# Kernel optimization log

Hardware: AMD Instinct MI355X
Metric: run time of the kernel (lower is better)

The kernel has to match this reference:

```python
import jax, jax.numpy as jnp
import numpy as np

N = 8192
D_IN = 3
D_K = 128
HID = 256
N_RES = 2
N_TRI = 2730
N_EDGE = 2048
EPS = float(jnp.finfo(jnp.float32).eps)  # torch RMSNorm default eps=None -> finfo eps


def setup_inputs() -> dict:
    key = jax.random.key(0)
    ks = jax.random.split(key, 16)
    std = 0.02
    inp = {
        "edge_features": jax.random.normal(ks[0], (N, D_IN), dtype=jnp.float32),
        "edge_ids": jax.random.randint(ks[1], (N,), 0, N_EDGE),
        "triangle_ids": jax.random.randint(ks[2], (N,), 0, N_TRI),
        # projections (stored as [in, out]; equivalent to torch Linear)
        "Wq": jax.random.normal(ks[3], (D_IN, D_K), dtype=jnp.float32) * std,
        "bq": jnp.zeros((D_K,), jnp.float32),
        "Wk": jax.random.normal(ks[4], (D_IN, D_K), dtype=jnp.float32) * std,
        "bk": jnp.zeros((D_K,), jnp.float32),
        "Wv": jax.random.normal(ks[5], (D_IN, D_K), dtype=jnp.float32) * std,
        "bv": jnp.zeros((D_K,), jnp.float32),
        # attention MLP: Linear(d_k, hid) -> N_RES ResBlocks -> Linear(hid, 1)
        "W0": jax.random.normal(ks[6], (D_K, HID), dtype=jnp.float32) * std,
        "b0": jnp.zeros((HID,), jnp.float32),
        "rms_w": jnp.ones((N_RES, HID), jnp.float32),
        "Wres": jax.random.normal(ks[7], (N_RES, HID, HID), dtype=jnp.float32) * std,
        "bres": jnp.zeros((N_RES, HID), jnp.float32),
        "Wout": jax.random.normal(ks[8], (HID, 1), dtype=jnp.float32) * std,
        "bout": jnp.zeros((1,), jnp.float32),
    }
    return inp


def _rmsnorm(x, g):
    ms = jnp.mean(x * x, axis=-1, keepdims=True)
    return x * jax.lax.rsqrt(ms + EPS) * g


def reference(edge_features, edge_ids, triangle_ids,
              Wq, bq, Wk, bk, Wv, bv,
              W0, b0, rms_w, Wres, bres, Wout, bout):
    q = edge_features @ Wq + bq          # [N, d_k]
    k = edge_features @ Wk + bk
    v = edge_features @ Wv + bv
    scores = (q @ k.T) / jnp.sqrt(jnp.float32(D_K))   # [N, N]
    mask = triangle_ids[:, None] == triangle_ids[None, :]
    scores = jnp.where(mask, scores, -jnp.inf)
    attn = jax.nn.softmax(scores, axis=1)             # every row has diag True
    attended = attn @ v                                # [N, d_k]
    # MLP with ResBlocks
    h = attended @ W0 + b0                             # [N, hid]
    for i in range(N_RES):
        h = h + jax.nn.relu(_rmsnorm(h, rms_w[i]) @ Wres[i] + bres[i])
    logits = (h @ Wout + bout)[:, 0]                   # [N]
    # scatter_softmax over edge_ids (dim=0)
    seg_max = jax.ops.segment_max(logits, edge_ids, num_segments=N_EDGE)
    ex = jnp.exp(logits - seg_max[edge_ids])
    seg_sum = jax.ops.segment_sum(ex, edge_ids, num_segments=N_EDGE)
    weights = ex / seg_sum[edge_ids]
    return weights
```

## Files before the change

### kernel.cpp

```cpp
#include <hip/hip_runtime.h>
#include <math.h>

#define N 8192
#define D_IN 3
#define D_K 128
#define HID 256
#define N_RES 2
#define N_TRI 2730
#define N_EDGE 2048
#define EPS 1.1920929e-07f

typedef unsigned short u16;
typedef unsigned int u32;
typedef float f32x4 __attribute__((ext_vector_type(4)));
typedef short s16x8 __attribute__((ext_vector_type(8)));

#define OFF_LOGITS   0
#define OFF_TRIOFF   32768
#define OFF_TRICNT   43776
#define OFF_MEMT     54784
#define OFF_EOFF     87552
#define OFF_ECNT     95744
#define OFF_MEME     103936
#define OFF_WPK      136704

__device__ __forceinline__ u16 f2bf(float f) {
    u32 u = __float_as_uint(f);
    u32 r = (u + 0x7fffu + ((u >> 16) & 1u)) >> 16;
    return (u16)r;
}
__device__ __forceinline__ u32 pack2bf(float a, float b) {
    return (u32)f2bf(a) | ((u32)f2bf(b) << 16);
}

__global__ __launch_bounds__(1024) void k_setup(
        const int* __restrict__ tri, const int* __restrict__ eids,
        const float* __restrict__ W0, const float* __restrict__ Wres,
        int* __restrict__ tri_off, int* __restrict__ tri_cnt, int* __restrict__ mem_t,
        int* __restrict__ e_off, int* __restrict__ e_cnt, int* __restrict__ mem_e,
        u16* __restrict__ Wpk) {
    if (blockIdx.x != 0) {
        int tg = (blockIdx.x - 1) * 1024 + threadIdx.x;
        int tile = tg >> 6, lane = tg & 63;
        int q = lane >> 4, c = lane & 15;
        u16 tmp[8];
        int dst;
        if (tile < 64) {
            int nt = tile >> 2, kt = tile & 3;
            int k0 = kt * 32 + q * 8, n = nt * 16 + c;
            dst = (tile * 64 + lane) * 8;
            #pragma unroll
            for (int j = 0; j < 8; ++j) tmp[j] = f2bf(W0[(k0 + j) * HID + n]);
        } else {
            int t2 = tile - 64;
            int r = t2 >> 7, tl = t2 & 127;
            int nt = tl >> 3, kt = tl & 7;
            int k0 = kt * 32 + q * 8, n = nt * 16 + c;
            dst = 32768 + r * 65536 + (tl * 64 + lane) * 8;
            const float* W = Wres + r * 65536;
            #pragma unroll
            for (int j = 0; j < 8; ++j) tmp[j] = f2bf(W[(k0 + j) * HID + n]);
        }
        *(s16x8*)&Wpk[dst] = *(s16x8*)tmp;
        return;
    }
    __shared__ int sc[4096];
    __shared__ int ec[2048];
    __shared__ int wp[16];
    const int t = threadIdx.x, lane = t & 63, wid = t >> 6;
    for (int i = t; i < 4096; i += 1024) sc[i] = 0;
    for (int i = t; i < 2048; i += 1024) ec[i] = 0;
    __syncthreads();
    for (int n = t; n < N; n += 1024) {
        atomicAdd(&sc[tri[n]], 1);
        atomicAdd(&ec[eids[n]], 1);
    }
    __syncthreads();
    int a0 = sc[t*4], a1 = sc[t*4+1], a2 = sc[t*4+2], a3 = sc[t*4+3];
    int c0 = a0, c1 = c0 + a1, c2 = c1 + a2, c3 = c2 + a3;
    int ts = c3;
    #pragma unroll
    for (int o = 1; o < 64; o <<= 1) { int u = __shfl_up(ts, o); if (lane >= o) ts += u; }
    if (lane == 63) wp[wid] = ts;
    __syncthreads();
    if (wid == 0) {
        int v = (lane < 16) ? wp[lane] : 0;
        #pragma unroll
        for (int o = 1; o < 16; o <<= 1) { int u = __shfl_up(v, o); if (lane >= o) v += u; }
        if (lane < 16) wp[lane] = v;
    }
    __syncthreads();
    {
        int wexcl = wid ? wp[wid - 1] : 0;
        int texcl = wexcl + ts - c3;
        int o0 = texcl, o1 = texcl + c0, o2 = texcl + c1, o3 = texcl + c2;
        if (t*4+0 < N_TRI) { tri_off[t*4+0] = o0; tri_cnt[t*4+0] = a0; }
        if (t*4+1 < N_TRI) { tri_off[t*4+1] = o1; tri_cnt[t*4+1] = a1; }
        if (t*4+2 < N_TRI) { tri_off[t*4+2] = o2; tri_cnt[t*4+2] = a2; }
        if (t*4+3 < N_TRI) { tri_off[t*4+3] = o3; tri_cnt[t*4+3] = a3; }
        sc[t*4+0] = o0; sc[t*4+1] = o1; sc[t*4+2] = o2; sc[t*4+3] = o3;
    }
    __syncthreads();
    int ea0 = ec[t*2], ea1 = ec[t*2+1];
    int f0 = ea0, f1 = f0 + ea1;
    int es = f1;
    #pragma unroll
    for (int o = 1; o < 64; o <<= 1) { int u = __shfl_up(es, o); if (lane >= o) es += u; }
    if (lane == 63) wp[wid] = es;
    __syncthreads();
    if (wid == 0) {
        int v = (lane < 16) ? wp[lane] : 0;
        #pragma unroll
        for (int o = 1; o < 16; o <<= 1) { int u = __shfl_up(v, o); if (lane >= o) v += u; }
        if (lane < 16) wp[lane] = v;
    }
    __syncthreads();
    {
        int wexcl = wid ? wp[wid - 1] : 0;
        int texcl = wexcl + es - f1;
        int eo0 = texcl, eo1 = texcl + f0;
        e_off[t*2+0] = eo0; e_cnt[t*2+0] = ea0;
        e_off[t*2+1] = eo1; e_cnt[t*2+1] = ea1;
        ec[t*2+0] = eo0; ec[t*2+1] = eo1;
    }
    __syncthreads();
    for (int n = t; n < N; n += 1024) {
        int p = atomicAdd(&sc[tri[n]], 1);
        mem_t[p] = n;
        int q2 = atomicAdd(&ec[eids[n]], 1);
        mem_e[q2] = n;
    }
}

__global__ __launch_bounds__(512) void k_fused(
        const float* __restrict__ ef, const int* __restrict__ tri,
        const float* __restrict__ Wq, const float* __restrict__ bq,
        const float* __restrict__ Wk, const float* __restrict__ bk,
        const float* __restrict__ Wv, const float* __restrict__ bv,
        const int* __restrict__ tri_off, const int* __restrict__ tri_cnt,
        const int* __restrict__ mem_t,
        const float* __restrict__ b0, const float* __restrict__ rms_w,
        const float* __restrict__ bres, const float* __restrict__ Wout,
        const float* __restrict__ bout, const u16* __restrict__ Wpk,
        float* __restrict__ logits) {
    __shared__ u16 X[16][264];
    __shared__ float red[8][16];
    const int tid = threadIdx.x;
    const int w = tid >> 6, lane = tid & 63;
    const int q = lane >> 4, c = lane & 15;
    const int base = blockIdx.x * 16;
    const int colb = w * 32 + c;

    {
        const int d0 = lane * 2, d1 = d0 + 1;
        float wq0a = Wq[d0], wq1a = Wq[D_K + d0], wq2a = Wq[2*D_K + d0], bqa = bq[d0];
        float wq0b = Wq[d1], wq1b = Wq[D_K + d1], wq2b = Wq[2*D_K + d1], bqb = bq[d1];
        float wk0a = Wk[d0], wk1a = Wk[D_K + d0], wk2a = Wk[2*D_K + d0], bka = bk[d0];
        float wk0b = Wk[d1], wk1b = Wk[D_K + d1], wk2b = Wk[2*D_K + d1], bkb = bk[d1];
        float wv0a = Wv[d0], wv1a = Wv[D_K + d0], wv2a = Wv[2*D_K + d0], bva = bv[d0];
        float wv0b = Wv[d1], wv1b = Wv[D_K + d1], wv2b = Wv[2*D_K + d1], bvb = bv[d1];
        const float scale = 0.08838834764831845f;

        #pragma unroll
        for (int rr = 0; rr < 2; ++rr) {
            int lrow = 2 * w + rr;
            int row = base + lrow;
            float e0 = ef[row*3+0], e1 = ef[row*3+1], e2 = ef[row*3+2];
            float qa = bqa + e0*wq0a + e1*wq1a + e2*wq2a;
            float qb = bqb + e0*wq0b + e1*wq1b + e2*wq2b;
            int tt = tri[row];
            int off = tri_off[tt], cnt = tri_cnt[tt];
            float m = -INFINITY, l = 0.f, acca = 0.f, accb = 0.f;
            for (int bs = 0; bs < cnt; bs += 64) {
                int nn = cnt - bs; if (nn > 64) nn = 64;
                float g0 = 0.f, g1 = 0.f, g2 = 0.f;
                if (lane < nn) {
                    int j = mem_t[off + bs + lane];
                    g0 = ef[j*3+0]; g1 = ef[j*3+1]; g2 = ef[j*3+2];
                }
                for (int ii = 0; ii < nn; ++ii) {
                    float h0 = __shfl(g0, ii), h1 = __shfl(g1, ii), h2 = __shfl(g2, ii);
                    float ka = bka + h0*wk0a + h1*wk1a + h2*wk2a;
                    float kb = bkb + h0*wk0b + h1*wk1b + h2*wk2b;
                    float p = qa * ka + qb * kb;
                    #pragma unroll
                    for (int o = 32; o > 0; o >>= 1) p += __shfl_xor(p, o);
                    float s = p * scale;
                    float va = bva + h0*wv0a + h1*wv1a + h2*wv2a;
                    float vb = bvb + h0*wv0b + h1*wv1b + h2*wv2b;
                    float mn = fmaxf(m, s);
                    float rs = expf(m - mn);
                    float ws = expf(s - mn);
                    l    = l * rs + ws;
                    acca = acca * rs + ws * va;
                    accb = accb * rs + ws * vb;
                    m = mn;
                }
            }
            float inv = 1.f / l;
            *(u32*)&X[lrow][d0] = pack2bf(acca * inv, accb * inv);
        }
    }
    __syncthreads();

    const s16x8* Bp = (const s16x8*)Wpk;
    float h[2][4];
    f32x4 acc[2];
    const f32x4 zero = {0.f, 0.f, 0.f, 0.f};

    #pragma unroll
    for (int nt = 0; nt < 2; ++nt) acc[nt] = zero;
    #pragma unroll
    for (int kt = 0; kt < 4; ++kt) {
        s16x8 a = *(const s16x8*)&X[c][kt * 32 + q * 8];
        #pragma unroll
        for (int nt = 0; nt < 2; ++nt) {
            s16x8 b = Bp[((w * 2 + nt) * 4 + kt) * 64 + lane];
            acc[nt] = __builtin_amdgcn_mfma_f32_16x16x32_bf16(a, b, acc[nt], 0, 0, 0);
        }
    }
    #pragma unroll
    for (int nt = 0; nt < 2; ++nt) {
        float bb = b0[colb + nt * 16];
        #pragma unroll
        for (int rg = 0; rg < 4; ++rg) h[nt][rg] = acc[nt][rg] + bb;
    }

    for (int ir = 0; ir < N_RES; ++ir) {
        float part[4];
        #pragma unroll
        for (int rg = 0; rg < 4; ++rg) {
            part[rg] = h[0][rg] * h[0][rg] + h[1][rg] * h[1][rg];
            #pragma unroll
            for (int o = 1; o < 16; o <<= 1) part[rg] += __shfl_xor(part[rg], o);
        }
        if (c == 0) {
            #pragma unroll
            for (int rg = 0; rg < 4; ++rg) red[w][q * 4 + rg] = part[rg];
        }
        __syncthreads();
        float sc4[4];
        #pragma unroll
        for (int rg = 0; rg < 4; ++rg) {
            int rr = q * 4 + rg;
            float ms = (red[0][rr] + red[1][rr] + red[2][rr] + red[3][rr]
                      + red[4][rr] + red[5][rr] + red[6][rr] + red[7][rr]) * (1.f / HID);
            sc4[rg] = rsqrtf(ms + EPS);
        }
        #pragma unroll
        for (int nt = 0; nt < 2; ++nt) {
            float gg = rms_w[ir * HID + colb + nt * 16];
            #pragma unroll
            for (int rg = 0; rg < 4; ++rg)
                X[q * 4 + rg][colb + nt * 16] = f2bf(h[nt][rg] * sc4[rg] * gg);
        }
        __syncthreads();

        const s16x8* Br = Bp + 4096 + ir * 8192;
        #pragma unroll
        for (int nt = 0; nt < 2; ++nt) acc[nt] = zero;
        #pragma unroll
        for (int kt = 0; kt < 8; ++kt) {
            s16x8 a = *(const s16x8*)&X[c][kt * 32 + q * 8];
            #pragma unroll
            for (int nt = 0; nt < 2; ++nt) {
                s16x8 b = Br[((w * 2 + nt) * 8 + kt) * 64 + lane];
                acc[nt] = __builtin_amdgcn_mfma_f32_16x16x32_bf16(a, b, acc[nt], 0, 0, 0);
            }
        }
        #pragma unroll
        for (int nt = 0; nt < 2; ++nt) {
            float bb = bres[ir * HID + colb + nt * 16];
            #pragma unroll
            for (int rg = 0; rg < 4; ++rg) h[nt][rg] += fmaxf(acc[nt][rg] + bb, 0.f);
        }
    }

    {
        float wo0 = Wout[colb], wo1 = Wout[colb + 16];
        float part[4];
        #pragma unroll
        for (int rg = 0; rg < 4; ++rg) {
            part[rg] = h[0][rg] * wo0 + h[1][rg] * wo1;
            #pragma unroll
            for (int o = 1; o < 16; o <<= 1) part[rg] += __shfl_xor(part[rg], o);
        }
        if (c == 0) {
            #pragma unroll
            for (int rg = 0; rg < 4; ++rg) red[w][q * 4 + rg] = part[rg];
        }
        __syncthreads();
        if (tid < 16) {
            float s = bout[0];
            #pragma unroll
            for (int w2 = 0; w2 < 8; ++w2) s += red[w2][tid];
            logits[base + tid] = s;
        }
    }
}

__global__ __launch_bounds__(256) void k_segsoft(
        const float* __restrict__ logits, const int* __restrict__ e_off,
        const int* __restrict__ e_cnt, const int* __restrict__ mem_e,
        float* __restrict__ out) {
    int e = (blockIdx.x * 256 + threadIdx.x) >> 6;
    int lane = threadIdx.x & 63;
    int off = e_off[e], cnt = e_cnt[e];
    float mx = -INFINITY;
    for (int i = lane; i < cnt; i += 64) mx = fmaxf(mx, logits[mem_e[off + i]]);
    #pragma unroll
    for (int o = 32; o > 0; o >>= 1) mx = fmaxf(mx, __shfl_xor(mx, o));
    float s = 0.f;
    for (int i = lane; i < cnt; i += 64) s += expf(logits[mem_e[off + i]] - mx);
    #pragma unroll
    for (int o = 32; o > 0; o >>= 1) s += __shfl_xor(s, o);
    float inv = 1.f / s;
    for (int i = lane; i < cnt; i += 64) {
        int m = mem_e[off + i];
        out[m] = expf(logits[m] - mx) * inv;
    }
}

extern "C" void kernel_launch(void* const* d_in, const int* in_sizes, int n_in,
                              void* d_out, int out_size, void* d_ws, size_t ws_size,
                              hipStream_t stream) {
    const float* ef   = (const float*)d_in[0];
    const int*   eids = (const int*)d_in[1];
    const int*   tri  = (const int*)d_in[2];
    const float* Wq = (const float*)d_in[3];
    const float* bq = (const float*)d_in[4];
    const float* Wk = (const float*)d_in[5];
    const float* bk = (const float*)d_in[6];
    const float* Wv = (const float*)d_in[7];
    const float* bv = (const float*)d_in[8];
    const float* W0 = (const float*)d_in[9];
    const float* b0 = (const float*)d_in[10];
    const float* rms_w = (const float*)d_in[11];
    const float* Wres  = (const float*)d_in[12];
    const float* bres  = (const float*)d_in[13];
    const float* Wout  = (const float*)d_in[14];
    const float* bout  = (const float*)d_in[15];
    float* out = (float*)d_out;

    char* ws = (char*)d_ws;
    float* logits  = (float*)(ws + OFF_LOGITS);
    int*   tri_off = (int*)(ws + OFF_TRIOFF);
    int*   tri_cnt = (int*)(ws + OFF_TRICNT);
    int*   mem_t   = (int*)(ws + OFF_MEMT);
    int*   e_off   = (int*)(ws + OFF_EOFF);
    int*   e_cnt   = (int*)(ws + OFF_ECNT);
    int*   mem_e   = (int*)(ws + OFF_MEME);
    u16*   Wpk     = (u16*)(ws + OFF_WPK);

    hipLaunchKernelGGL(k_setup, dim3(21), dim3(1024), 0, stream,
                       tri, eids, W0, Wres,
                       tri_off, tri_cnt, mem_t, e_off, e_cnt, mem_e, Wpk);
    hipLaunchKernelGGL(k_fused, dim3(N / 16), dim3(512), 0, stream,
                       ef, tri, Wq, bq, Wk, bk, Wv, bv,
                       tri_off, tri_cnt, mem_t,
                       b0, rms_w, bres, Wout, bout, Wpk, logits);
    hipLaunchKernelGGL(k_segsoft, dim3(N_EDGE / 4), dim3(256), 0, stream,
                       logits, e_off, e_cnt, mem_e, out);
}
```

Baseline: 120.0 us.

## Fold Q/K/V and W0 projections into low-rank precomputed constants

Because D_IN is 3, the attention score reduces to a 3x3 bilinear form, and attn@v@W0 reduces to averaging the 3-dim edge features and then applying a precomputed 3x256 matrix. The setup kernel now computes these small matrices (Wq·Wkᵀ terms, Wv·W0, and the folded bias). The fused kernel then runs attention in 3 dimensions using 32-lane halves with per-chunk softmax and no per-element 64-lane reductions, and replaces the first MFMA GEMM with a rank-3 FMA. This removes most of the attention ALU and shuffle work. It changes rounding, since the first layer now runs in fp32 instead of bf16.

```diff
diff --git a/kernel.cpp b/kernel.cpp
--- a/kernel.cpp
+++ b/kernel.cpp
@@ -23,44 +23,71 @@
 #define OFF_ECNT     95744
 #define OFF_MEME     103936
 #define OFF_WPK      136704
+#define OFF_WV0      398848
+#define OFF_B0P      401920
+#define OFF_ATTC     402944
 
 __device__ __forceinline__ u16 f2bf(float f) {
     u32 u = __float_as_uint(f);
     u32 r = (u + 0x7fffu + ((u >> 16) & 1u)) >> 16;
     return (u16)r;
 }
-__device__ __forceinline__ u32 pack2bf(float a, float b) {
-    return (u32)f2bf(a) | ((u32)f2bf(b) << 16);
-}
 
 __global__ __launch_bounds__(1024) void k_setup(
         const int* __restrict__ tri, const int* __restrict__ eids,
-        const float* __restrict__ W0, const float* __restrict__ Wres,
+        const float* __restrict__ Wq, const float* __restrict__ bq,
+        const float* __restrict__ Wk, const float* __restrict__ bk,
+        const float* __restrict__ Wv, const float* __restrict__ bv,
+        const float* __restrict__ W0, const float* __restrict__ b0,
+        const float* __restrict__ Wres,
         int* __restrict__ tri_off, int* __restrict__ tri_cnt, int* __restrict__ mem_t,
         int* __restrict__ e_off, int* __restrict__ e_cnt, int* __restrict__ mem_e,
-        u16* __restrict__ Wpk) {
+        u16* __restrict__ Wpk, float* __restrict__ Wv0, float* __restrict__ b0p,
+        float* __restrict__ attc) {
+    if (blockIdx.x == 17) {
+        int t = threadIdx.x;
+        if (t < 256) {
+            float a0 = 0.f, a1 = 0.f, a2 = 0.f, ab = 0.f;
+            for (int d = 0; d < D_K; ++d) {
+                float wc = W0[d * HID + t];
+                a0 += Wv[d] * wc;
+                a1 += Wv[D_K + d] * wc;
+                a2 += Wv[2 * D_K + d] * wc;
+                ab += bv[d] * wc;
+            }
+            Wv0[t] = a0; Wv0[256 + t] = a1; Wv0[512 + t] = a2;
+            b0p[t] = ab + b0[t];
+        } else if (t < 272) {
+            int idx = t - 256;
+            float acc = 0.f;
+            if (idx < 9) {
+                int a = idx / 3, b = idx % 3;
+                for (int d = 0; d < D_K; ++d) acc += Wq[a * D_K + d] * Wk[b * D_K + d];
+            } else if (idx < 12) {
+                int a = idx - 9;
+                for (int d = 0; d < D_K; ++d) acc += Wq[a * D_K + d] * bk[d];
+            } else if (idx < 15) {
+                int b = idx - 12;
+                for (int d = 0; d < D_K; ++d) acc += bq[d] * Wk[b * D_K + d];
+            } else {
+                for (int d = 0; d < D_K; ++d) acc += bq[d] * bk[d];
+            }
+            attc[idx] = acc;
+        }
+        return;
+    }
     if (blockIdx.x != 0) {
         int tg = (blockIdx.x - 1) * 1024 + threadIdx.x;
         int tile = tg >> 6, lane = tg & 63;
         int q = lane >> 4, c = lane & 15;
+        int r = tile >> 7, tl = tile & 127;
+        int nt = tl >> 3, kt = tl & 7;
+        int k0 = kt * 32 + q * 8, n = nt * 16 + c;
+        const float* W = Wres + r * 65536;
         u16 tmp[8];
-        int dst;
-        if (tile < 64) {
-            int nt = tile >> 2, kt = tile & 3;
-            int k0 = kt * 32 + q * 8, n = nt * 16 + c;
-            dst = (tile * 64 + lane) * 8;
-            #pragma unroll
-            for (int j = 0; j < 8; ++j) tmp[j] = f2bf(W0[(k0 + j) * HID + n]);
-        } else {
-            int t2 = tile - 64;
-            int r = t2 >> 7, tl = t2 & 127;
-            int nt = tl >> 3, kt = tl & 7;
-            int k0 = kt * 32 + q * 8, n = nt * 16 + c;
-            dst = 32768 + r * 65536 + (tl * 64 + lane) * 8;
-            const float* W = Wres + r * 65536;
-            #pragma unroll
-            for (int j = 0; j < 8; ++j) tmp[j] = f2bf(W[(k0 + j) * HID + n]);
-        }
+        #pragma unroll
+        for (int j = 0; j < 8; ++j) tmp[j] = f2bf(W[(k0 + j) * HID + n]);
+        int dst = r * 65536 + (tl * 64 + lane) * 8;
         *(s16x8*)&Wpk[dst] = *(s16x8*)tmp;
         return;
     }
@@ -134,17 +161,16 @@
 
 __global__ __launch_bounds__(512) void k_fused(
         const float* __restrict__ ef, const int* __restrict__ tri,
-        const float* __restrict__ Wq, const float* __restrict__ bq,
-        const float* __restrict__ Wk, const float* __restrict__ bk,
-        const float* __restrict__ Wv, const float* __restrict__ bv,
         const int* __restrict__ tri_off, const int* __restrict__ tri_cnt,
         const int* __restrict__ mem_t,
-        const float* __restrict__ b0, const float* __restrict__ rms_w,
+        const float* __restrict__ attc, const float* __restrict__ Wv0,
+        const float* __restrict__ b0p, const float* __restrict__ rms_w,
         const float* __restrict__ bres, const float* __restrict__ Wout,
         const float* __restrict__ bout, const u16* __restrict__ Wpk,
         float* __restrict__ logits) {
     __shared__ u16 X[16][264];
     __shared__ float red[8][16];
+    __shared__ float ebar[16][4];
     const int tid = threadIdx.x;
     const int w = tid >> 6, lane = tid & 63;
     const int q = lane >> 4, c = lane & 15;
@@ -152,53 +178,53 @@
     const int colb = w * 32 + c;
 
     {
-        const int d0 = lane * 2, d1 = d0 + 1;
-        float wq0a = Wq[d0], wq1a = Wq[D_K + d0], wq2a = Wq[2*D_K + d0], bqa = bq[d0];
-        float wq0b = Wq[d1], wq1b = Wq[D_K + d1], wq2b = Wq[2*D_K + d1], bqb = bq[d1];
-        float wk0a = Wk[d0], wk1a = Wk[D_K + d0], wk2a = Wk[2*D_K + d0], bka = bk[d0];
-        float wk0b = Wk[d1], wk1b = Wk[D_K + d1], wk2b = Wk[2*D_K + d1], bkb = bk[d1];
-        float wv0a = Wv[d0], wv1a = Wv[D_K + d0], wv2a = Wv[2*D_K + d0], bva = bv[d0];
-        float wv0b = Wv[d1], wv1b = Wv[D_K + d1], wv2b = Wv[2*D_K + d1], bvb = bv[d1];
         const float scale = 0.08838834764831845f;
-
-        #pragma unroll
-        for (int rr = 0; rr < 2; ++rr) {
-            int lrow = 2 * w + rr;
-            int row = base + lrow;
-            float e0 = ef[row*3+0], e1 = ef[row*3+1], e2 = ef[row*3+2];
-            float qa = bqa + e0*wq0a + e1*wq1a + e2*wq2a;
-            float qb = bqb + e0*wq0b + e1*wq1b + e2*wq2b;
-            int tt = tri[row];
-            int off = tri_off[tt], cnt = tri_cnt[tt];
-            float m = -INFINITY, l = 0.f, acca = 0.f, accb = 0.f;
-            for (int bs = 0; bs < cnt; bs += 64) {
-                int nn = cnt - bs; if (nn > 64) nn = 64;
-                float g0 = 0.f, g1 = 0.f, g2 = 0.f;
-                if (lane < nn) {
-                    int j = mem_t[off + bs + lane];
-                    g0 = ef[j*3+0]; g1 = ef[j*3+1]; g2 = ef[j*3+2];
-                }
-                for (int ii = 0; ii < nn; ++ii) {
-                    float h0 = __shfl(g0, ii), h1 = __shfl(g1, ii), h2 = __shfl(g2, ii);
-                    float ka = bka + h0*wk0a + h1*wk1a + h2*wk2a;
-                    float kb = bkb + h0*wk0b + h1*wk1b + h2*wk2b;
-                    float p = qa * ka + qb * kb;
-                    #pragma unroll
-                    for (int o = 32; o > 0; o >>= 1) p += __shfl_xor(p, o);
-                    float s = p * scale;
-                    float va = bva + h0*wv0a + h1*wv1a + h2*wv2a;
-                    float vb = bvb + h0*wv0b + h1*wv1b + h2*wv2b;
-                    float mn = fmaxf(m, s);
-                    float rs = expf(m - mn);
-                    float ws = expf(s - mn);
-                    l    = l * rs + ws;
-                    acca = acca * rs + ws * va;
-                    accb = accb * rs + ws * vb;
-                    m = mn;
-                }
-            }
+        const int half = lane >> 5;
+        const int i = lane & 31;
+        const int lrow = 2 * w + half;
+        const int row = base + lrow;
+        float e0 = ef[row*3+0], e1 = ef[row*3+1], e2 = ef[row*3+2];
+        float t0 = (e0*attc[0] + e1*attc[3] + e2*attc[6] + attc[12]) * scale;
+        float t1 = (e0*attc[1] + e1*attc[4] + e2*attc[7] + attc[13]) * scale;
+        float t2 = (e0*attc[2] + e1*attc[5] + e2*attc[8] + attc[14]) * scale;
+        float tb = (e0*attc[9] + e1*attc[10] + e2*attc[11] + attc[15]) * scale;
+        int tt = tri[row];
+        int off = tri_off[tt], cnt = tri_cnt[tt];
+        float m = -INFINITY, l = 0.f, sa0 = 0.f, sa1 = 0.f, sa2 = 0.f;
+        for (int bs = 0; bs < cnt; bs += 32) {
+            int nn = cnt - bs; if (nn > 32) nn = 32;
+            float f0 = 0.f, f1 = 0.f, f2 = 0.f, s = -INFINITY;
+            if (i < nn) {
+                int j = mem_t[off + bs + i];
+                f0 = ef[j*3+0]; f1 = ef[j*3+1]; f2 = ef[j*3+2];
+                s = tb + t0*f0 + t1*f1 + t2*f2;
+            }
+            float m1 = s;
+            #pragma unroll
+            for (int o = 16; o > 0; o >>= 1) m1 = fmaxf(m1, __shfl_xor(m1, o));
+            float p = (i < nn) ? __expf(s - m1) : 0.f;
+            float pl = p, p0 = p * f0, p1 = p * f1, p2 = p * f2;
+            #pragma unroll
+            for (int o = 16; o > 0; o >>= 1) {
+                pl += __shfl_xor(pl, o);
+                p0 += __shfl_xor(p0, o);
+                p1 += __shfl_xor(p1, o);
+                p2 += __shfl_xor(p2, o);
+            }
+            float mn = fmaxf(m, m1);
+            float ra = __expf(m - mn);
+            float rb = __expf(m1 - mn);
+            l   = l   * ra + pl * rb;
+            sa0 = sa0 * ra + p0 * rb;
+            sa1 = sa1 * ra + p1 * rb;
+            sa2 = sa2 * ra + p2 * rb;
+            m = mn;
+        }
+        if (i == 0) {
             float inv = 1.f / l;
-            *(u32*)&X[lrow][d0] = pack2bf(acca * inv, accb * inv);
+            ebar[lrow][0] = sa0 * inv;
+            ebar[lrow][1] = sa1 * inv;
+            ebar[lrow][2] = sa2 * inv;
         }
     }
     __syncthreads();
@@ -209,21 +235,14 @@
     const f32x4 zero = {0.f, 0.f, 0.f, 0.f};
 
     #pragma unroll
-    for (int nt = 0; nt < 2; ++nt) acc[nt] = zero;
-    #pragma unroll
-    for (int kt = 0; kt < 4; ++kt) {
-        s16x8 a = *(const s16x8*)&X[c][kt * 32 + q * 8];
-        #pragma unroll
-        for (int nt = 0; nt < 2; ++nt) {
-            s16x8 b = Bp[((w * 2 + nt) * 4 + kt) * 64 + lane];
-            acc[nt] = __builtin_amdgcn_mfma_f32_16x16x32_bf16(a, b, acc[nt], 0, 0, 0);
-        }
-    }
-    #pragma unroll
     for (int nt = 0; nt < 2; ++nt) {
-        float bb = b0[colb + nt * 16];
-        #pragma unroll
-        for (int rg = 0; rg < 4; ++rg) h[nt][rg] = acc[nt][rg] + bb;
+        int col = colb + nt * 16;
+        float w0 = Wv0[col], w1 = Wv0[256 + col], w2 = Wv0[512 + col], bb = b0p[col];
+        #pragma unroll
+        for (int rg = 0; rg < 4; ++rg) {
+            int rr = q * 4 + rg;
+            h[nt][rg] = bb + ebar[rr][0]*w0 + ebar[rr][1]*w1 + ebar[rr][2]*w2;
+        }
     }
 
     for (int ir = 0; ir < N_RES; ++ir) {
@@ -256,7 +275,7 @@
         }
         __syncthreads();
 
-        const s16x8* Br = Bp + 4096 + ir * 8192;
+        const s16x8* Br = Bp + ir * 8192;
         #pragma unroll
         for (int nt = 0; nt < 2; ++nt) acc[nt] = zero;
         #pragma unroll
@@ -351,14 +370,17 @@
     int*   e_cnt   = (int*)(ws + OFF_ECNT);
     int*   mem_e   = (int*)(ws + OFF_MEME);
     u16*   Wpk     = (u16*)(ws + OFF_WPK);
-
-    hipLaunchKernelGGL(k_setup, dim3(21), dim3(1024), 0, stream,
-                       tri, eids, W0, Wres,
-                       tri_off, tri_cnt, mem_t, e_off, e_cnt, mem_e, Wpk);
+    float* Wv0     = (float*)(ws + OFF_WV0);
+    float* b0p     = (float*)(ws + OFF_B0P);
+    float* attc    = (float*)(ws + OFF_ATTC);
+
+    hipLaunchKernelGGL(k_setup, dim3(18), dim3(1024), 0, stream,
+                       tri, eids, Wq, bq, Wk, bk, Wv, bv, W0, b0, Wres,
+                       tri_off, tri_cnt, mem_t, e_off, e_cnt, mem_e,
+                       Wpk, Wv0, b0p, attc);
     hipLaunchKernelGGL(k_fused, dim3(N / 16), dim3(512), 0, stream,
-                       ef, tri, Wq, bq, Wk, bk, Wv, bv,
-                       tri_off, tri_cnt, mem_t,
-                       b0, rms_w, bres, Wout, bout, Wpk, logits);
+                       ef, tri, tri_off, tri_cnt, mem_t,
+                       attc, Wv0, b0p, rms_w, bres, Wout, bout, Wpk, logits);
     hipLaunchKernelGGL(k_segsoft, dim3(N_EDGE / 4), dim3(256), 0, stream,
                        logits, e_off, e_cnt, mem_e, out);
 }
```

After: 112.6 us. 1.07x faster.
